# Optimization experiments

Measured on AMD Instinct MI355X. Metric: run time of the kernel, lower is better.

Reference implementation:

```python
import jax, jax.numpy as jnp
import numpy as np

# ---- static config (matches init_kwargs / input_specs) ----
MODEL_CONTEXT_LEN = 4096
BLOCK_SIZE = 16
NUM_Q_HEADS = 32
NUM_KV_HEADS = 8
HEAD_DIM = 128
ROPE_BASE = 10000.0
B = 8
NUM_PAST = 4613                                   # context_len - 1, same for all seqs
END_BNUM = NUM_PAST // BLOCK_SIZE                 # 288
REM = NUM_PAST % BLOCK_SIZE                       # 5
START_BNUM = (NUM_PAST - MODEL_CONTEXT_LEN) // BLOCK_SIZE + 2  # 34
CUR_POS = MODEL_CONTEXT_LEN - 1                   # 4095 (capped decode position)
BLOCKS_PER_SEQ = END_BNUM + 1                     # 289
NUM_BLOCKS = B * BLOCKS_PER_SEQ                   # 2312


def rope(pos, x):
    """NeoX-style rotary. pos: [T] int; x: [..., T, H, D]."""
    half = HEAD_DIM // 2
    inv = 1.0 / (ROPE_BASE ** (jnp.arange(half, dtype=jnp.float32) / half))
    freqs = pos.astype(jnp.float32)[:, None] * inv        # [T, half]
    cos = jnp.cos(freqs)[:, None, :]                      # [T, 1, half]
    sin = jnp.sin(freqs)[:, None, :]
    x1, x2 = jnp.split(x, 2, axis=-1)
    return jnp.concatenate([x1 * cos - x2 * sin, x2 * cos + x1 * sin], axis=-1)


def setup_inputs() -> dict:
    key = jax.random.key(0)
    ks = jax.random.split(key, 7)
    q = jax.random.normal(ks[0], (B, NUM_Q_HEADS * HEAD_DIM), jnp.float32)
    k = jax.random.normal(ks[1], (B, NUM_KV_HEADS * HEAD_DIM), jnp.float32)
    v = jax.random.normal(ks[2], (B, NUM_KV_HEADS * HEAD_DIM), jnp.float32)
    positions = jnp.full((B,), NUM_PAST, dtype=jnp.int32)
    context_lens = jnp.full((B,), NUM_PAST + 1, dtype=jnp.int32)
    # distinct physical blocks per sequence (paged layout)
    block_tables = jnp.arange(NUM_BLOCKS, dtype=jnp.int32).reshape(B, BLOCKS_PER_SEQ)
    # cache stores UN-rotated keys (module writes k_original); layout [nblk, bs, Hk, D]
    key_cache = jax.random.normal(ks[3], (NUM_BLOCKS, BLOCK_SIZE, NUM_KV_HEADS, HEAD_DIM), jnp.float32) * 0.5
    value_cache = jax.random.normal(ks[4], (NUM_BLOCKS, BLOCK_SIZE, NUM_KV_HEADS, HEAD_DIM), jnp.float32) * 0.5
    W_o = jax.random.normal(ks[5], (NUM_Q_HEADS * HEAD_DIM, NUM_Q_HEADS * HEAD_DIM), jnp.float32) * 0.02
    return {"q": q, "k": k, "v": v, "positions": positions, "context_lens": context_lens,
            "block_tables": block_tables, "key_cache": key_cache, "value_cache": value_cache, "W_o": W_o}


def reference(q, k, v, positions, context_lens, block_tables, key_cache, value_cache, W_o):
    # Decode path of StreamingAttentionSink, context > model_context_len:
    # gather sink block + sliding-window blocks, re-apply rotary at shifted
    # positions, attend with q/k roped at capped position, project output.
    # positions for re-roped past keys: sink tokens 0..bs-1, window tokens
    # 2*bs-1-rem .. model_context_len-2 (matches the torch code's pos arange).
    pos_sink = np.arange(BLOCK_SIZE)
    pos_win = np.arange(2 * BLOCK_SIZE - 1 - REM, MODEL_CONTEXT_LEN - 1)
    POS = jnp.asarray(np.concatenate([pos_sink, pos_win]), dtype=jnp.int32)  # [4085]

    qh = q.reshape(B, NUM_Q_HEADS, HEAD_DIM)
    kh = k.reshape(B, NUM_KV_HEADS, HEAD_DIM)
    vh = v.reshape(B, NUM_KV_HEADS, HEAD_DIM)

    # phys_bnums = [block_table[0]] + block_table[start:end]  -> [B, 255]
    phys = jnp.concatenate([block_tables[:, :1], block_tables[:, START_BNUM:END_BNUM]], axis=1)
    full_k = key_cache[phys].reshape(B, -1, NUM_KV_HEADS, HEAD_DIM)       # [B, 4080, Hk, D]
    rem_k = key_cache[block_tables[:, END_BNUM], :REM]                     # [B, 5, Hk, D]
    past_k = jnp.concatenate([full_k, rem_k], axis=1)                      # [B, 4085, Hk, D]
    full_v = value_cache[phys].reshape(B, -1, NUM_KV_HEADS, HEAD_DIM)
    rem_v = value_cache[block_tables[:, END_BNUM], :REM]
    past_v = jnp.concatenate([full_v, rem_v], axis=1)

    past_k = rope(POS, past_k)  # re-apply rotary to shifted sink/window keys

    cur = jnp.array([CUR_POS], dtype=jnp.int32)
    q_rot = rope(cur, qh[:, None, :, :])[:, 0]   # [B, H, D] at capped position
    k_rot = rope(cur, kh[:, None, :, :])[:, 0]   # [B, Hk, D]

    keys = jnp.concatenate([past_k, k_rot[:, None]], axis=1)   # [B, 4086, Hk, D]
    vals = jnp.concatenate([past_v, vh[:, None]], axis=1)

    # GQA attention (group = 4 q-heads per kv-head)
    G = NUM_Q_HEADS // NUM_KV_HEADS
    qg = q_rot.reshape(B, NUM_KV_HEADS, G, HEAD_DIM)
    scale = 1.0 / np.sqrt(HEAD_DIM).astype(np.float32)
    scores = jnp.einsum('bhgd,bthd->bhgt', qg, keys) * scale
    probs = jax.nn.softmax(scores, axis=-1)
    attn = jnp.einsum('bhgt,bthd->bhgd', probs, vals).reshape(B, NUM_Q_HEADS * HEAD_DIM)
    return attn @ W_o
```

## Files before the change

### kernel.cpp

```cpp
#include <hip/hip_runtime.h>
#include <math.h>

#define NB 8
#define NQH 32
#define NKVH 8
#define HD 128
#define GQ 4
#define T_TOT 4086
#define T_PAST 4085
#define SPLITS 32
#define TCHUNK 128
#define TILE 32
#define PPAD 130
#define BPS 289
#define LOG2_10K_OVER_64 0.2076205059304601f
#define SCALE 0.08838834764831843f
#define LOG2E 1.4426950408889634f

#define PART_ATTN_OFF 0
#define PART_ATTN_SZ  (64 * GQ * SPLITS * PPAD)
#define ATTN_OFF      PART_ATTN_SZ

__device__ __forceinline__ void rope_cs(float posf, int j, float& cs, float& sn)
{
    const float INV2PI = 0.15915494309189535f;
    const float P1 = 6.28125f;
    const float P2 = 0.0019354820251464844f;
    const float P3 = -1.748455600075e-7f;
    float inv  = __builtin_amdgcn_exp2f(-(float)j * LOG2_10K_OVER_64);
    float freq = posf * inv;
    float n    = rintf(freq * INV2PI);
    float red  = fmaf(-n, P1, freq);
    red        = fmaf(-n, P2, red);
    red        = fmaf(-n, P3, red);
    float rev  = red * INV2PI;
    sn = __builtin_amdgcn_sinf(rev);
    cs = __builtin_amdgcn_cosf(rev);
}

__global__ __launch_bounds__(256, 6) void attn_partial_kernel(
    const float* __restrict__ q,
    const int* __restrict__ bt, const float* __restrict__ kc, const float* __restrict__ vc,
    float* __restrict__ part)
{
    __shared__ float kt[TILE][132];
    __shared__ float qs[GQ][132];
    __shared__ float sc[GQ][36];
    __shared__ unsigned int offr[TCHUNK];
    __shared__ int posr[TCHUNK];
    __shared__ float lred[4][GQ];

    const int tid  = threadIdx.x;
    const int bh   = blockIdx.x;
    const int s    = blockIdx.y;
    const int b    = bh >> 3, h = bh & 7;
    const int lane = tid & 63, w = tid >> 6;
    const int t0   = s * TCHUNK;
    const int* btb = bt + b * BPS;

    if (tid < TCHUNK) {
        int tg = t0 + tid;
        unsigned int off = 0u; int pos = 0;
        if (tg < T_PAST) {
            int bti, rr;
            if (tg < 16)        { bti = 0;              rr = tg;        pos = tg;      }
            else if (tg < 4080) { bti = 33 + (tg >> 4); rr = tg & 15;   pos = tg + 10; }
            else                { bti = 288;            rr = tg - 4080; pos = tg + 10; }
            off = (unsigned int)(((btb[bti] * 16 + rr) * NKVH + h) * HD);
        }
        offr[tid] = off; posr[tid] = pos;
    }
    {
        const float* qp = q + (size_t)b * (NQH * HD) + (size_t)h * (GQ * HD);
        for (int e = tid; e < GQ * HD; e += 256) {
            int g = e >> 7, d = e & 127, j = d & 63;
            float cs, sn; rope_cs(4095.0f, j, cs, sn);
            float x1 = qp[g * HD + j], x2 = qp[g * HD + j + 64];
            qs[g][d] = ((d < 64) ? (x1 * cs - x2 * sn) : (x2 * cs + x1 * sn)) * SCALE;
        }
    }

    float acc0 = 0.f, acc1 = 0.f, l_run = 0.f;
    const int g_s = (lane >> 4) & 3, tl_s = (lane >> 1) & 7, hf = lane & 1;
    const int gp = w >> 1, cc = (w & 1) * 64 + lane;
    const float* vcc = vc + cc;

    for (int tb = 0; tb < TCHUNK; tb += TILE) {
        __syncthreads();

        #pragma unroll
        for (int it = 0; it < 2; ++it) {
            int e = tid + it * 256;
            int row = e >> 4, c4 = (e & 15) << 2;
            unsigned int off = offr[tb + row];
            float posf = (float)posr[tb + row];
            const float* ks = kc + off;
            float4 k1 = *(const float4*)(ks + c4);
            float4 k2 = *(const float4*)(ks + 64 + c4);
            float4 lo, hi; float cs, sn;
            rope_cs(posf, c4 + 0, cs, sn); lo.x = k1.x*cs - k2.x*sn; hi.x = k2.x*cs + k1.x*sn;
            rope_cs(posf, c4 + 1, cs, sn); lo.y = k1.y*cs - k2.y*sn; hi.y = k2.y*cs + k1.y*sn;
            rope_cs(posf, c4 + 2, cs, sn); lo.z = k1.z*cs - k2.z*sn; hi.z = k2.z*cs + k1.z*sn;
            rope_cs(posf, c4 + 3, cs, sn); lo.w = k1.w*cs - k2.w*sn; hi.w = k2.w*cs + k1.w*sn;
            *(float4*)&kt[row][c4]      = lo;
            *(float4*)&kt[row][64 + c4] = hi;
        }
        __syncthreads();

        {
            int t = w * 8 + tl_s;
            const float* kr = &kt[t][hf * 64];
            const float* qr = &qs[g_s][hf * 64];
            float dot = 0.f;
            #pragma unroll
            for (int j4 = 0; j4 < 16; ++j4) {
                float4 kk = *(const float4*)(kr + (j4 << 2));
                float4 qq = *(const float4*)(qr + (j4 << 2));
                dot += kk.x*qq.x + kk.y*qq.y + kk.z*qq.z + kk.w*qq.w;
            }
            dot += __shfl_xor(dot, 1);
            int tg = t0 + tb + t;
            float p = (tg < T_PAST) ? __builtin_amdgcn_exp2f(dot * LOG2E) : 0.f;
            l_run += p;
            if (hf == 0) sc[g_s][t] = p;
        }
        __syncthreads();

        #pragma unroll
        for (int t4 = 0; t4 < 8; ++t4) {
            float4 p40 = *(const float4*)&sc[2*gp][t4 << 2];
            float4 p41 = *(const float4*)&sc[2*gp + 1][t4 << 2];
            int t = t4 << 2;
            float v0 = vcc[offr[tb + t]];
            float v1 = vcc[offr[tb + t + 1]];
            float v2 = vcc[offr[tb + t + 2]];
            float v3 = vcc[offr[tb + t + 3]];
            acc0 += p40.x*v0 + p40.y*v1 + p40.z*v2 + p40.w*v3;
            acc1 += p41.x*v0 + p41.y*v1 + p41.z*v2 + p41.w*v3;
        }
    }

    float lr = l_run;
    lr += __shfl_xor(lr, 1); lr += __shfl_xor(lr, 2);
    lr += __shfl_xor(lr, 4); lr += __shfl_xor(lr, 8);
    if ((lane & 15) == 0) lred[w][lane >> 4] = lr;
    __syncthreads();

    float* pp0 = part + ((size_t)(bh * GQ + 2*gp    ) * SPLITS + s) * PPAD;
    float* pp1 = part + ((size_t)(bh * GQ + 2*gp + 1) * SPLITS + s) * PPAD;
    pp0[cc] = acc0;
    pp1[cc] = acc1;
    if (tid < GQ) {
        float l = 0.5f * (lred[0][tid] + lred[1][tid] + lred[2][tid] + lred[3][tid]);
        part[((size_t)(bh * GQ + tid) * SPLITS + s) * PPAD + 129] = l;
    }
}

__global__ __launch_bounds__(256) void attn_reduce_kernel(
    const float* __restrict__ part,
    const float* __restrict__ q, const float* __restrict__ k, const float* __restrict__ v,
    float* __restrict__ attn, float* __restrict__ out)
{
    int bh = blockIdx.x;
    int tid = threadIdx.x;
    int g = tid >> 6, lane = tid & 63;
    int b = bh >> 3, h = bh & 7;

    *(float2*)(out + (size_t)(bh * 256 + tid) * 2) = make_float2(0.f, 0.f);

    const float* qp = q + (size_t)b * (NQH * HD) + (size_t)(h * GQ + g) * HD;
    const float* kp = k + (size_t)(b * NKVH + h) * HD;
    float cs, sn; rope_cs(4095.0f, lane, cs, sn);
    float q1 = qp[lane], q2 = qp[lane + 64];
    float k1 = kp[lane], k2 = kp[lane + 64];
    float qr1 = q1*cs - q2*sn, qr2 = q2*cs + q1*sn;
    float kr1 = k1*cs - k2*sn, kr2 = k2*cs + k1*sn;
    float dot = qr1*kr1 + qr2*kr2;
    dot += __shfl_xor(dot, 1);  dot += __shfl_xor(dot, 2);
    dot += __shfl_xor(dot, 4);  dot += __shfl_xor(dot, 8);
    dot += __shfl_xor(dot, 16); dot += __shfl_xor(dot, 32);
    float p_cur = __builtin_amdgcn_exp2f(dot * SCALE * LOG2E);

    const float* pg = part + (size_t)(bh * GQ + g) * SPLITS * PPAD;
    float accl = 0.f, acch = 0.f, l = 0.f;
    #pragma unroll 8
    for (int s = 0; s < SPLITS; ++s) {
        l    += pg[s * PPAD + 129];
        accl += pg[s * PPAD + lane];
        acch += pg[s * PPAD + lane + 64];
    }
    const float* vp = v + (size_t)(b * NKVH + h) * HD;
    accl += p_cur * vp[lane];
    acch += p_cur * vp[lane + 64];
    l += p_cur;
    float inv_l = 1.0f / l;
    size_t base = (size_t)b * 4096 + (size_t)(h * GQ + g) * 128;
    attn[base + lane]      = accl * inv_l;
    attn[base + lane + 64] = acch * inv_l;
}

__global__ __launch_bounds__(256) void gemm_partial_kernel(
    const float* __restrict__ attn, const float* __restrict__ Wo,
    float* __restrict__ out)
{
    __shared__ float a_s[NB][256];
    __shared__ float red[4][NB][128];
    int tid = threadIdx.x;
    int lane = tid & 63, w = tid >> 6;
    int jt = blockIdx.x;
    int is = blockIdx.y;
    int i0 = is * 256;
    int c  = jt * 128 + lane * 2;
    for (int e = tid; e < NB * 256; e += 256) {
        int bb = e >> 8, i = e & 255;
        a_s[bb][i] = attn[(size_t)bb * 4096 + i0 + i];
    }
    __syncthreads();
    float accx[NB] = {}, accy[NB] = {};
    const float* wp = Wo + (size_t)(i0 + w * 64) * 4096 + c;
    #pragma unroll 8
    for (int ii = 0; ii < 64; ++ii) {
        float2 wv = *(const float2*)(wp + (size_t)ii * 4096);
        int il = w * 64 + ii;
        #pragma unroll
        for (int bb = 0; bb < NB; ++bb) {
            float a = a_s[bb][il];
            accx[bb] += a * wv.x;
            accy[bb] += a * wv.y;
        }
    }
    #pragma unroll
    for (int bb = 0; bb < NB; ++bb) {
        red[w][bb][lane * 2]     = accx[bb];
        red[w][bb][lane * 2 + 1] = accy[bb];
    }
    __syncthreads();
    for (int e = tid; e < NB * 128; e += 256) {
        int bb = e >> 7, l = e & 127;
        float sum = red[0][bb][l] + red[1][bb][l] + red[2][bb][l] + red[3][bb][l];
        atomicAdd(&out[(size_t)bb * 4096 + jt * 128 + l], sum);
    }
}

extern "C" void kernel_launch(void* const* d_in, const int* in_sizes, int n_in,
                              void* d_out, int out_size, void* d_ws, size_t ws_size,
                              hipStream_t stream) {
    const float* q  = (const float*)d_in[0];
    const float* k  = (const float*)d_in[1];
    const float* v  = (const float*)d_in[2];
    const int*   bt = (const int*)d_in[5];
    const float* kc = (const float*)d_in[6];
    const float* vc = (const float*)d_in[7];
    const float* Wo = (const float*)d_in[8];
    float* out = (float*)d_out;
    float* ws  = (float*)d_ws;

    float* part_attn = ws + PART_ATTN_OFF;
    float* attn      = ws + ATTN_OFF;

    attn_partial_kernel<<<dim3(64, SPLITS), 256, 0, stream>>>(q, bt, kc, vc, part_attn);
    attn_reduce_kernel<<<64, 256, 0, stream>>>(part_attn, q, k, v, attn, out);
    gemm_partial_kernel<<<dim3(32, 16), 256, 0, stream>>>(attn, Wo, out);
}
```

Before: 377.9 us.

## Software-pipeline K/V tile loads through registers and stage V in LDS

Prefetches the next tile's K and V rows into registers while the current tile is being computed. V is staged into a new shared-memory tile with coalesced float4 loads, replacing the scattered per-element global reads in the PV loop. Hoists the per-column RoPE inverse frequencies out of the loop, replaces __syncthreads with a raw LDS-wait-plus-barrier, and drops the occupancy hint from launch bounds. This adds register pressure and extra LDS plus a barrier per tile, which may lower occupancy.

Measured after the change: 396.8 us. +5.0%, slower.

```diff
diff --git a/kernel.cpp b/kernel.cpp
--- a/kernel.cpp
+++ b/kernel.cpp
@@ -21,13 +21,15 @@
 #define PART_ATTN_SZ  (64 * GQ * SPLITS * PPAD)
 #define ATTN_OFF      PART_ATTN_SZ
 
-__device__ __forceinline__ void rope_cs(float posf, int j, float& cs, float& sn)
+#define LDSBAR() do { asm volatile("s_waitcnt lgkmcnt(0)" ::: "memory"); \
+                      __builtin_amdgcn_s_barrier(); } while (0)
+
+__device__ __forceinline__ void rope_cs_inv(float posf, float inv, float& cs, float& sn)
 {
     const float INV2PI = 0.15915494309189535f;
     const float P1 = 6.28125f;
     const float P2 = 0.0019354820251464844f;
     const float P3 = -1.748455600075e-7f;
-    float inv  = __builtin_amdgcn_exp2f(-(float)j * LOG2_10K_OVER_64);
     float freq = posf * inv;
     float n    = rintf(freq * INV2PI);
     float red  = fmaf(-n, P1, freq);
@@ -38,12 +40,19 @@
     cs = __builtin_amdgcn_cosf(rev);
 }
 
-__global__ __launch_bounds__(256, 6) void attn_partial_kernel(
+__device__ __forceinline__ void rope_cs(float posf, int j, float& cs, float& sn)
+{
+    float inv = __builtin_amdgcn_exp2f(-(float)j * LOG2_10K_OVER_64);
+    rope_cs_inv(posf, inv, cs, sn);
+}
+
+__global__ __launch_bounds__(256) void attn_partial_kernel(
     const float* __restrict__ q,
     const int* __restrict__ bt, const float* __restrict__ kc, const float* __restrict__ vc,
     float* __restrict__ part)
 {
     __shared__ float kt[TILE][132];
+    __shared__ float vt[TILE][128];
     __shared__ float qs[GQ][132];
     __shared__ float sc[GQ][36];
     __shared__ unsigned int offr[TCHUNK];
@@ -80,32 +89,62 @@
         }
     }
 
+    const int kc4  = (tid & 15) << 2;
+    const int krow0 = tid >> 4;
+    float invj[4];
+    #pragma unroll
+    for (int jj = 0; jj < 4; ++jj)
+        invj[jj] = __builtin_amdgcn_exp2f(-(float)(kc4 + jj) * LOG2_10K_OVER_64);
+
     float acc0 = 0.f, acc1 = 0.f, l_run = 0.f;
     const int g_s = (lane >> 4) & 3, tl_s = (lane >> 1) & 7, hf = lane & 1;
     const int gp = w >> 1, cc = (w & 1) * 64 + lane;
-    const float* vcc = vc + cc;
-
+
+    LDSBAR();
+
+    float4 pk1[2], pk2[2], pv[4];
+    auto prefetch = [&](int tb) {
+        #pragma unroll
+        for (int it = 0; it < 2; ++it) {
+            unsigned int off = offr[tb + krow0 + it * 16];
+            const float* ks = kc + off;
+            pk1[it] = *(const float4*)(ks + kc4);
+            pk2[it] = *(const float4*)(ks + 64 + kc4);
+        }
+        #pragma unroll
+        for (int it = 0; it < 4; ++it) {
+            int e = tid + it * 256;
+            int row = e >> 5, c4 = (e & 31) << 2;
+            pv[it] = *(const float4*)(vc + offr[tb + row] + c4);
+        }
+    };
+
+    prefetch(0);
+
+    #pragma unroll
     for (int tb = 0; tb < TCHUNK; tb += TILE) {
-        __syncthreads();
-
         #pragma unroll
         for (int it = 0; it < 2; ++it) {
+            int row = krow0 + it * 16;
+            float posf = (float)posr[tb + row];
+            float4 k1 = pk1[it], k2 = pk2[it];
+            float4 lo, hi; float cs, sn;
+            rope_cs_inv(posf, invj[0], cs, sn); lo.x = k1.x*cs - k2.x*sn; hi.x = k2.x*cs + k1.x*sn;
+            rope_cs_inv(posf, invj[1], cs, sn); lo.y = k1.y*cs - k2.y*sn; hi.y = k2.y*cs + k1.y*sn;
+            rope_cs_inv(posf, invj[2], cs, sn); lo.z = k1.z*cs - k2.z*sn; hi.z = k2.z*cs + k1.z*sn;
+            rope_cs_inv(posf, invj[3], cs, sn); lo.w = k1.w*cs - k2.w*sn; hi.w = k2.w*cs + k1.w*sn;
+            *(float4*)&kt[row][kc4]      = lo;
+            *(float4*)&kt[row][64 + kc4] = hi;
+        }
+        #pragma unroll
+        for (int it = 0; it < 4; ++it) {
             int e = tid + it * 256;
-            int row = e >> 4, c4 = (e & 15) << 2;
-            unsigned int off = offr[tb + row];
-            float posf = (float)posr[tb + row];
-            const float* ks = kc + off;
-            float4 k1 = *(const float4*)(ks + c4);
-            float4 k2 = *(const float4*)(ks + 64 + c4);
-            float4 lo, hi; float cs, sn;
-            rope_cs(posf, c4 + 0, cs, sn); lo.x = k1.x*cs - k2.x*sn; hi.x = k2.x*cs + k1.x*sn;
-            rope_cs(posf, c4 + 1, cs, sn); lo.y = k1.y*cs - k2.y*sn; hi.y = k2.y*cs + k1.y*sn;
-            rope_cs(posf, c4 + 2, cs, sn); lo.z = k1.z*cs - k2.z*sn; hi.z = k2.z*cs + k1.z*sn;
-            rope_cs(posf, c4 + 3, cs, sn); lo.w = k1.w*cs - k2.w*sn; hi.w = k2.w*cs + k1.w*sn;
-            *(float4*)&kt[row][c4]      = lo;
-            *(float4*)&kt[row][64 + c4] = hi;
-        }
-        __syncthreads();
+            int row = e >> 5, c4 = (e & 31) << 2;
+            *(float4*)&vt[row][c4] = pv[it];
+        }
+        LDSBAR();
+
+        if (tb + TILE < TCHUNK) prefetch(tb + TILE);
 
         {
             int t = w * 8 + tl_s;
@@ -124,27 +163,25 @@
             l_run += p;
             if (hf == 0) sc[g_s][t] = p;
         }
-        __syncthreads();
+        LDSBAR();
 
         #pragma unroll
         for (int t4 = 0; t4 < 8; ++t4) {
             float4 p40 = *(const float4*)&sc[2*gp][t4 << 2];
             float4 p41 = *(const float4*)&sc[2*gp + 1][t4 << 2];
             int t = t4 << 2;
-            float v0 = vcc[offr[tb + t]];
-            float v1 = vcc[offr[tb + t + 1]];
-            float v2 = vcc[offr[tb + t + 2]];
-            float v3 = vcc[offr[tb + t + 3]];
+            float v0 = vt[t][cc], v1 = vt[t+1][cc], v2 = vt[t+2][cc], v3 = vt[t+3][cc];
             acc0 += p40.x*v0 + p40.y*v1 + p40.z*v2 + p40.w*v3;
             acc1 += p41.x*v0 + p41.y*v1 + p41.z*v2 + p41.w*v3;
         }
+        LDSBAR();
     }
 
     float lr = l_run;
     lr += __shfl_xor(lr, 1); lr += __shfl_xor(lr, 2);
     lr += __shfl_xor(lr, 4); lr += __shfl_xor(lr, 8);
     if ((lane & 15) == 0) lred[w][lane >> 4] = lr;
-    __syncthreads();
+    LDSBAR();
 
     float* pp0 = part + ((size_t)(bh * GQ + 2*gp    ) * SPLITS + s) * PPAD;
     float* pp1 = part + ((size_t)(bh * GQ + 2*gp + 1) * SPLITS + s) * PPAD;
```

## Restructure partial attention into per-wave register pipeline without LDS tiles

Applied to the files above, without the earlier changes.

The partial attention kernel now gives each wave its own 32 tokens. Each half-wave processes one token per step, keeping K and V as float2 values in registers and prefetching the next token's K/V one step ahead. Dot products are reduced with cross-lane shuffles instead of LDS tiles and repeated block barriers, and the RoPE inverse frequencies are precomputed once per lane. Per-wave partial accumulators are combined through shared memory at the end. This removes most __syncthreads and LDS traffic but adds shuffle-reduction cost and register pressure, and drops the occupancy hint.

After: 367.9 us. -2.6%, faster.

```diff
diff --git a/kernel.cpp b/kernel.cpp
--- a/kernel.cpp
+++ b/kernel.cpp
@@ -6,11 +6,9 @@
 #define NKVH 8
 #define HD 128
 #define GQ 4
-#define T_TOT 4086
 #define T_PAST 4085
 #define SPLITS 32
 #define TCHUNK 128
-#define TILE 32
 #define PPAD 130
 #define BPS 289
 #define LOG2_10K_OVER_64 0.2076205059304601f
@@ -21,13 +19,12 @@
 #define PART_ATTN_SZ  (64 * GQ * SPLITS * PPAD)
 #define ATTN_OFF      PART_ATTN_SZ
 
-__device__ __forceinline__ void rope_cs(float posf, int j, float& cs, float& sn)
+__device__ __forceinline__ void rope_cs_inv(float posf, float inv, float& cs, float& sn)
 {
     const float INV2PI = 0.15915494309189535f;
     const float P1 = 6.28125f;
     const float P2 = 0.0019354820251464844f;
     const float P3 = -1.748455600075e-7f;
-    float inv  = __builtin_amdgcn_exp2f(-(float)j * LOG2_10K_OVER_64);
     float freq = posf * inv;
     float n    = rintf(freq * INV2PI);
     float red  = fmaf(-n, P1, freq);
@@ -38,120 +35,147 @@
     cs = __builtin_amdgcn_cosf(rev);
 }
 
-__global__ __launch_bounds__(256, 6) void attn_partial_kernel(
+__device__ __forceinline__ void rope_cs(float posf, int j, float& cs, float& sn)
+{
+    float inv = __builtin_amdgcn_exp2f(-(float)j * LOG2_10K_OVER_64);
+    rope_cs_inv(posf, inv, cs, sn);
+}
+
+__global__ __launch_bounds__(256) void attn_partial_kernel(
     const float* __restrict__ q,
     const int* __restrict__ bt, const float* __restrict__ kc, const float* __restrict__ vc,
     float* __restrict__ part)
 {
-    __shared__ float kt[TILE][132];
-    __shared__ float qs[GQ][132];
-    __shared__ float sc[GQ][36];
-    __shared__ unsigned int offr[TCHUNK];
-    __shared__ int posr[TCHUNK];
-    __shared__ float lred[4][GQ];
+    __shared__ float red[4][GQ][128];
+    __shared__ float lredb[4][GQ];
 
     const int tid  = threadIdx.x;
     const int bh   = blockIdx.x;
     const int s    = blockIdx.y;
     const int b    = bh >> 3, h = bh & 7;
     const int lane = tid & 63, w = tid >> 6;
-    const int t0   = s * TCHUNK;
+    const int hl   = lane & 31;
+    const int half = lane >> 5;
+    const int t0w  = s * TCHUNK + w * 32;
     const int* btb = bt + b * BPS;
 
-    if (tid < TCHUNK) {
-        int tg = t0 + tid;
-        unsigned int off = 0u; int pos = 0;
-        if (tg < T_PAST) {
+    unsigned int offv = 0u; int posv = 0;
+    {
+        int tokl = t0w + hl;
+        if (tokl < T_PAST) {
             int bti, rr;
-            if (tg < 16)        { bti = 0;              rr = tg;        pos = tg;      }
-            else if (tg < 4080) { bti = 33 + (tg >> 4); rr = tg & 15;   pos = tg + 10; }
-            else                { bti = 288;            rr = tg - 4080; pos = tg + 10; }
-            off = (unsigned int)(((btb[bti] * 16 + rr) * NKVH + h) * HD);
+            if (tokl < 16)        { bti = 0;                rr = tokl;        }
+            else if (tokl < 4080) { bti = 33 + (tokl >> 4); rr = tokl & 15;   }
+            else                  { bti = 288;              rr = tokl - 4080; }
+            offv = (unsigned int)(((btb[bti] * 16 + rr) * NKVH + h) * HD);
+            posv = (tokl < 16) ? tokl : tokl + 10;
         }
-        offr[tid] = off; posr[tid] = pos;
-    }
+    }
+
+    const float inv0 = __builtin_amdgcn_exp2f(-(float)(2 * hl)     * LOG2_10K_OVER_64);
+    const float inv1 = __builtin_amdgcn_exp2f(-(float)(2 * hl + 1) * LOG2_10K_OVER_64);
+
+    float2 qa[GQ], qb[GQ];
     {
-        const float* qp = q + (size_t)b * (NQH * HD) + (size_t)h * (GQ * HD);
-        for (int e = tid; e < GQ * HD; e += 256) {
-            int g = e >> 7, d = e & 127, j = d & 63;
-            float cs, sn; rope_cs(4095.0f, j, cs, sn);
-            float x1 = qp[g * HD + j], x2 = qp[g * HD + j + 64];
-            qs[g][d] = ((d < 64) ? (x1 * cs - x2 * sn) : (x2 * cs + x1 * sn)) * SCALE;
+        const float* qbase = q + (size_t)b * (NQH * HD) + (size_t)h * (GQ * HD);
+        float cq0, sq0, cq1, sq1;
+        rope_cs_inv(4095.0f, inv0, cq0, sq0);
+        rope_cs_inv(4095.0f, inv1, cq1, sq1);
+        #pragma unroll
+        for (int g = 0; g < GQ; ++g) {
+            float2 xa = *(const float2*)(qbase + g * HD + 2 * hl);
+            float2 xb = *(const float2*)(qbase + g * HD + 2 * hl + 64);
+            qa[g].x = (xa.x * cq0 - xb.x * sq0) * SCALE;
+            qb[g].x = (xb.x * cq0 + xa.x * sq0) * SCALE;
+            qa[g].y = (xa.y * cq1 - xb.y * sq1) * SCALE;
+            qb[g].y = (xb.y * cq1 + xa.y * sq1) * SCALE;
         }
     }
 
-    float acc0 = 0.f, acc1 = 0.f, l_run = 0.f;
-    const int g_s = (lane >> 4) & 3, tl_s = (lane >> 1) & 7, hf = lane & 1;
-    const int gp = w >> 1, cc = (w & 1) * 64 + lane;
-    const float* vcc = vc + cc;
-
-    for (int tb = 0; tb < TCHUNK; tb += TILE) {
-        __syncthreads();
-
+    float2 accl[GQ] = {}, acch[GQ] = {};
+    float  lr[GQ]   = {};
+
+#define AB_BODY(K1C,K2C,V1C,V2C, K1N,K2N,V1N,V2N, I, NI)                      \
+    {                                                                          \
+        unsigned int noff_ = __shfl(offv, 2 * (NI) + half);                    \
+        const float* kn_ = kc + noff_ + 2 * hl;                                \
+        const float* vn_ = vc + noff_ + 2 * hl;                                \
+        K1N = *(const float2*)kn_;        K2N = *(const float2*)(kn_ + 64);    \
+        V1N = *(const float2*)vn_;        V2N = *(const float2*)(vn_ + 64);    \
+        float posf_ = (float)__shfl(posv, 2 * (I) + half);                     \
+        float cs0_, sn0_, cs1_, sn1_;                                          \
+        rope_cs_inv(posf_, inv0, cs0_, sn0_);                                  \
+        rope_cs_inv(posf_, inv1, cs1_, sn1_);                                  \
+        float r1x_ = K1C.x * cs0_ - K2C.x * sn0_;                              \
+        float r2x_ = K2C.x * cs0_ + K1C.x * sn0_;                              \
+        float r1y_ = K1C.y * cs1_ - K2C.y * sn1_;                              \
+        float r2y_ = K2C.y * cs1_ + K1C.y * sn1_;                              \
+        float d_[GQ];                                                          \
+        _Pragma("unroll")                                                      \
+        for (int g = 0; g < GQ; ++g)                                           \
+            d_[g] = r1x_ * qa[g].x + r1y_ * qa[g].y                            \
+                  + r2x_ * qb[g].x + r2y_ * qb[g].y;                           \
+        _Pragma("unroll")                                                      \
+        for (int m_ = 1; m_ <= 16; m_ <<= 1) {                                 \
+            _Pragma("unroll")                                                  \
+            for (int g = 0; g < GQ; ++g) d_[g] += __shfl_xor(d_[g], m_);       \
+        }                                                                      \
+        bool valid_ = (t0w + 2 * (I) + half) < T_PAST;                         \
+        _Pragma("unroll")                                                      \
+        for (int g = 0; g < GQ; ++g) {                                         \
+            float p_ = valid_ ? __builtin_amdgcn_exp2f(d_[g] * LOG2E) : 0.f;   \
+            lr[g] += p_;                                                       \
+            accl[g].x = fmaf(p_, V1C.x, accl[g].x);                            \
+            accl[g].y = fmaf(p_, V1C.y, accl[g].y);                            \
+            acch[g].x = fmaf(p_, V2C.x, acch[g].x);                            \
+            acch[g].y = fmaf(p_, V2C.y, acch[g].y);                            \
+        }                                                                      \
+    }
+
+    float2 k1a, k2a, v1a, v2a, k1b, k2b, v1b, v2b;
+    {
+        unsigned int off0 = __shfl(offv, half);
+        const float* kp = kc + off0 + 2 * hl;
+        const float* vp = vc + off0 + 2 * hl;
+        k1a = *(const float2*)kp;       k2a = *(const float2*)(kp + 64);
+        v1a = *(const float2*)vp;       v2a = *(const float2*)(vp + 64);
+    }
+
+    #pragma unroll 1
+    for (int i = 0; i < 16; i += 2) {
+        AB_BODY(k1a, k2a, v1a, v2a, k1b, k2b, v1b, v2b, i, i + 1);
+        int ni2 = (i + 2 < 16) ? i + 2 : 15;
+        AB_BODY(k1b, k2b, v1b, v2b, k1a, k2a, v1a, v2a, i + 1, ni2);
+    }
+#undef AB_BODY
+
+    #pragma unroll
+    for (int g = 0; g < GQ; ++g) {
+        accl[g].x += __shfl_xor(accl[g].x, 32);
+        accl[g].y += __shfl_xor(accl[g].y, 32);
+        acch[g].x += __shfl_xor(acch[g].x, 32);
+        acch[g].y += __shfl_xor(acch[g].y, 32);
+        lr[g]     += __shfl_xor(lr[g], 32);
+    }
+
+    #pragma unroll
+    for (int g = 0; g < GQ; ++g) {
+        float2 st = (half == 0) ? accl[g] : acch[g];
+        *(float2*)&red[w][g][2 * hl + half * 64] = st;
+    }
+    if (lane == 0) {
         #pragma unroll
-        for (int it = 0; it < 2; ++it) {
-            int e = tid + it * 256;
-            int row = e >> 4, c4 = (e & 15) << 2;
-            unsigned int off = offr[tb + row];
-            float posf = (float)posr[tb + row];
-            const float* ks = kc + off;
-            float4 k1 = *(const float4*)(ks + c4);
-            float4 k2 = *(const float4*)(ks + 64 + c4);
-            float4 lo, hi; float cs, sn;
-            rope_cs(posf, c4 + 0, cs, sn); lo.x = k1.x*cs - k2.x*sn; hi.x = k2.x*cs + k1.x*sn;
-            rope_cs(posf, c4 + 1, cs, sn); lo.y = k1.y*cs - k2.y*sn; hi.y = k2.y*cs + k1.y*sn;
-            rope_cs(posf, c4 + 2, cs, sn); lo.z = k1.z*cs - k2.z*sn; hi.z = k2.z*cs + k1.z*sn;
-            rope_cs(posf, c4 + 3, cs, sn); lo.w = k1.w*cs - k2.w*sn; hi.w = k2.w*cs + k1.w*sn;
-            *(float4*)&kt[row][c4]      = lo;
-            *(float4*)&kt[row][64 + c4] = hi;
-        }
-        __syncthreads();
-
-        {
-            int t = w * 8 + tl_s;
-            const float* kr = &kt[t][hf * 64];
-            const float* qr = &qs[g_s][hf * 64];
-            float dot = 0.f;
-            #pragma unroll
-            for (int j4 = 0; j4 < 16; ++j4) {
-                float4 kk = *(const float4*)(kr + (j4 << 2));
-                float4 qq = *(const float4*)(qr + (j4 << 2));
-                dot += kk.x*qq.x + kk.y*qq.y + kk.z*qq.z + kk.w*qq.w;
-            }
-            dot += __shfl_xor(dot, 1);
-            int tg = t0 + tb + t;
-            float p = (tg < T_PAST) ? __builtin_amdgcn_exp2f(dot * LOG2E) : 0.f;
-            l_run += p;
-            if (hf == 0) sc[g_s][t] = p;
-        }
-        __syncthreads();
-
-        #pragma unroll
-        for (int t4 = 0; t4 < 8; ++t4) {
-            float4 p40 = *(const float4*)&sc[2*gp][t4 << 2];
-            float4 p41 = *(const float4*)&sc[2*gp + 1][t4 << 2];
-            int t = t4 << 2;
-            float v0 = vcc[offr[tb + t]];
-            float v1 = vcc[offr[tb + t + 1]];
-            float v2 = vcc[offr[tb + t + 2]];
-            float v3 = vcc[offr[tb + t + 3]];
-            acc0 += p40.x*v0 + p40.y*v1 + p40.z*v2 + p40.w*v3;
-            acc1 += p41.x*v0 + p41.y*v1 + p41.z*v2 + p41.w*v3;
-        }
-    }
-
-    float lr = l_run;
-    lr += __shfl_xor(lr, 1); lr += __shfl_xor(lr, 2);
-    lr += __shfl_xor(lr, 4); lr += __shfl_xor(lr, 8);
-    if ((lane & 15) == 0) lred[w][lane >> 4] = lr;
+        for (int g = 0; g < GQ; ++g) lredb[w][g] = lr[g];
+    }
     __syncthreads();
 
-    float* pp0 = part + ((size_t)(bh * GQ + 2*gp    ) * SPLITS + s) * PPAD;
-    float* pp1 = part + ((size_t)(bh * GQ + 2*gp + 1) * SPLITS + s) * PPAD;
-    pp0[cc] = acc0;
-    pp1[cc] = acc1;
+    for (int e = tid; e < GQ * 128; e += 256) {
+        int g = e >> 7, d = e & 127;
+        float sum = red[0][g][d] + red[1][g][d] + red[2][g][d] + red[3][g][d];
+        part[((size_t)(bh * GQ + g) * SPLITS + s) * PPAD + d] = sum;
+    }
     if (tid < GQ) {
-        float l = 0.5f * (lred[0][tid] + lred[1][tid] + lred[2][tid] + lred[3][tid]);
+        float l = lredb[0][tid] + lredb[1][tid] + lredb[2][tid] + lredb[3][tid];
         part[((size_t)(bh * GQ + tid) * SPLITS + s) * PPAD + 129] = l;
     }
 }
```
